# Optimization experiments

Measured on AMD Instinct MI355X. Metric: run time of the kernel, lower is better.

## Reference

```python
import jax, jax.numpy as jnp
import numpy as np

EPS = 1e-6


def _mp_match(reps, att, kernel):
    """BiMPM multi-perspective match.
    reps: (B,L,D); att: (B,L,D) or (B,1,D); kernel: (M,D).
    Returns (B,L,1+M): [tanh(sum(reps*att)), tanh(sum_d reps*kernel_m*att)].
    """
    prod = reps * att                                   # (B,L,D)
    cos = jnp.tanh(jnp.sum(prod, axis=-1, keepdims=True))   # (B,L,1)
    mp = jnp.tanh(jnp.einsum('bld,md->blm', prod, kernel))  # (B,L,M)
    return jnp.concatenate([cos, mp], axis=-1)


def setup_inputs() -> dict:
    key = jax.random.key(0)
    ks = jax.random.split(key, 12)
    B, Llt, Lrt, D, M, A = 32, 128, 128, 512, 64, 128
    H = D // 2
    u = lambda k, shape: jax.random.uniform(k, shape, jnp.float32, -0.05, 0.05)  # keras 'uniform' init
    return {
        'reps_lt': jax.random.normal(ks[0], (B, Llt, D), jnp.float32),
        'h_lt_fw': jax.random.normal(ks[1], (B, H), jnp.float32),
        'h_lt_bw': jax.random.normal(ks[2], (B, H), jnp.float32),
        'reps_rt': jax.random.normal(ks[3], (B, Lrt, D), jnp.float32),
        'h_rt_fw': jax.random.normal(ks[4], (B, H), jnp.float32),
        'h_rt_bw': jax.random.normal(ks[5], (B, H), jnp.float32),
        'kernel_full': u(ks[6], (M, D)),
        'kernel_mpool': u(ks[7], (M, D)),
        'attn_w1': u(ks[8], (D, A)),
        'diag_w': u(ks[9], (A,)),
        'kernel_att': u(ks[10], (M, D)),
        'kernel_maxatt': u(ks[11], (M, D)),
    }


def reference(reps_lt, h_lt_fw, h_lt_bw, reps_rt, h_rt_fw, h_rt_bw,
              kernel_full, kernel_mpool, attn_w1, diag_w,
              kernel_att, kernel_maxatt):
    # ---- full match: each left timestep vs last BiLSTM state of right ----
    h_rt = jnp.concatenate([h_rt_fw, h_rt_bw], axis=-1)[:, None, :]  # (B,1,D)
    full = _mp_match(reps_lt, h_rt, kernel_full)                     # (B,Ll,1+M)

    # ---- max-pooling match ----
    # t[b,r,l,m] = tanh(sum_d R[b,r,d]*K[m,d]*L[b,l,d]); max over right positions r
    r_scaled = jnp.einsum('brd,md->brmd', reps_rt, kernel_mpool)     # (B,Lr,M,D)
    t = jnp.tanh(jnp.einsum('brmd,bld->brlm', r_scaled, reps_lt))    # (B,Lr,Ll,M)
    mpool = jnp.max(t, axis=1)                                       # (B,Ll,M)

    # ---- attentive match ----
    a_lt = jnp.tanh(reps_lt @ attn_w1) * diag_w                      # (B,Ll,A)
    a_rt = jnp.tanh(reps_rt @ attn_w1)                               # (B,Lr,A)
    scores = jnp.einsum('bla,bra->blr', a_lt, a_rt)                  # (B,Ll,Lr)
    probs = jax.nn.softmax(scores, axis=-1)
    att = jnp.einsum('blr,brd->bld', probs, reps_rt)                 # (B,Ll,D)
    attentive = _mp_match(reps_lt, att, kernel_att)                  # (B,Ll,1+M)

    # ---- max-attentive match ----
    num = jnp.einsum('bld,brd->blr', reps_lt, reps_rt)
    n_lt = jnp.sqrt(jnp.maximum(jnp.sum(reps_lt * reps_lt, -1), EPS))[:, :, None]
    n_rt = jnp.sqrt(jnp.maximum(jnp.sum(reps_rt * reps_rt, -1), EPS))[:, None, :]
    rel = num / n_rt / n_lt                                          # (B,Ll,Lr)
    idx = jnp.argmax(rel, axis=2)                                    # (B,Ll) int
    max_att = jnp.take_along_axis(reps_rt, idx[:, :, None], axis=1)  # (B,Ll,D)
    maxatt = _mp_match(reps_lt, max_att, kernel_maxatt)              # (B,Ll,1+M)

    return jnp.concatenate([full, mpool, attentive, maxatt], axis=-1)  # (B,Ll,3+4M)
```

## Files before the change

### kernel.cpp

```cpp
#include <hip/hip_runtime.h>
#include <hip/hip_bf16.h>
#include <math.h>
#include <stdint.h>

typedef __attribute__((ext_vector_type(8))) short short8;
typedef __attribute__((ext_vector_type(4))) float float4v;

#define DEV static __device__ __forceinline__

DEV float bflo(unsigned int u) { union { unsigned int i; float f; } v; v.i = u << 16; return v.f; }
DEV float bfhi(unsigned int u) { union { unsigned int i; float f; } v; v.i = u & 0xffff0000u; return v.f; }
DEV unsigned short f2bf(float f) {
    union { float f; unsigned int i; } v; v.f = f;
    unsigned int x = v.i;
    return (unsigned short)((x + 0x7fffu + ((x >> 16) & 1u)) >> 16);
}
DEV unsigned int pack2(float a, float b) { return (unsigned int)f2bf(a) | ((unsigned int)f2bf(b) << 16); }
#if __has_builtin(__builtin_amdgcn_cvt_pk_bf16_f32)
DEV unsigned int pack2_fast(float a, float b) {
    typedef __attribute__((ext_vector_type(2))) short short2v;
    short2v r = __builtin_amdgcn_cvt_pk_bf16_f32(a, b);
    union { short2v s; unsigned int u; } v; v.s = r; return v.u;
}
#else
DEV unsigned int pack2_fast(float a, float b) { return pack2(a, b); }
#endif
DEV void unpack8(uint4 u, float* f) {
    f[0]=bflo(u.x); f[1]=bfhi(u.x); f[2]=bflo(u.y); f[3]=bfhi(u.y);
    f[4]=bflo(u.z); f[5]=bfhi(u.z); f[6]=bflo(u.w); f[7]=bfhi(u.w);
}

DEV void async16(const unsigned short* g, unsigned short* l) {
    __builtin_amdgcn_global_load_lds(
        (const __attribute__((address_space(1))) unsigned int*)g,
        (__attribute__((address_space(3))) unsigned int*)l, 16, 0, 0);
}

__global__ __launch_bounds__(256) void prep_kernel(const float* __restrict__ lt,
                                                   const float* __restrict__ rt,
                                                   const float* __restrict__ kf,
                                                   const float* __restrict__ kmp,
                                                   const float* __restrict__ ka,
                                                   const float* __restrict__ km,
                                                   const float* __restrict__ w1,
                                                   unsigned short* __restrict__ ltb,
                                                   unsigned short* __restrict__ rtb,
                                                   unsigned short* __restrict__ kb,
                                                   unsigned short* __restrict__ w1t,
                                                   double* __restrict__ rsq) {
    __shared__ double ws2[2][2];
    __shared__ float tile[32][33];
    int bid = blockIdx.x, t = threadIdx.x;
    if (bid < 4096) {
        bool isRt = bid >= 2048;
        int rl = t >> 7;
        int c  = t & 127;
        int row = (isRt ? (bid - 2048) : bid) * 2 + rl;
        const float* src = (isRt ? rt : lt) + (size_t)row * 512;
        unsigned short* dst = (isRt ? rtb : ltb) + (size_t)row * 512;
        float4 v = *(const float4*)(src + c * 4);
        ushort4 o;
        o.x = f2bf(v.x); o.y = f2bf(v.y); o.z = f2bf(v.z); o.w = f2bf(v.w);
        *(ushort4*)(dst + c * 4) = o;
        if (isRt) {
            double s = (double)v.x * v.x + (double)v.y * v.y
                     + (double)v.z * v.z + (double)v.w * v.w;
            #pragma unroll
            for (int off = 1; off < 64; off <<= 1) s += __shfl_xor(s, off, 64);
            if ((c & 63) == 0) ws2[rl][c >> 6] = s;
            __syncthreads();
            if (c == 0) rsq[row] = 1.0 / sqrt(ws2[rl][0] + ws2[rl][1]);
        }
    } else if (bid < 4224) {
        int kbk = bid - 4096;
        int ksel = kbk >> 5;
        const float* src = (ksel == 0) ? kf : (ksel == 1) ? kmp : (ksel == 2) ? ka : km;
        int off = (kbk & 31) * 1024 + t * 4;
        float4 v = *(const float4*)(src + off);
        ushort4 o;
        o.x = f2bf(v.x); o.y = f2bf(v.y); o.z = f2bf(v.z); o.w = f2bf(v.w);
        *(ushort4*)(kb + ksel * 32768 + off) = o;
    } else {
        int b2 = bid - 4224;
        int d0 = (b2 & 15) * 32, a0 = (b2 >> 4) * 32;
        int r = t >> 5, c = t & 31;
        #pragma unroll
        for (int i = 0; i < 32; i += 8)
            tile[r + i][c] = w1[(size_t)(d0 + r + i) * 128 + a0 + c];
        __syncthreads();
        #pragma unroll
        for (int i = 0; i < 32; i += 8)
            w1t[(size_t)(a0 + r + i) * 512 + d0 + c] = f2bf(tile[c][r + i]);
    }
}

__global__ __launch_bounds__(256, 3) void uber_kernel(
        const unsigned short* __restrict__ ltb,
        const unsigned short* __restrict__ rtb,
        const unsigned short* __restrict__ kmb,
        const unsigned short* __restrict__ w1t,
        const float* __restrict__ diag,
        unsigned short* __restrict__ a_all,
        const float* __restrict__ ltf,
        const float* __restrict__ rtf,
        const double* __restrict__ rsq,
        int* __restrict__ idxout,
        float* __restrict__ out) {
    __shared__ __align__(16) unsigned char smem[52224];
    int bx = blockIdx.x;
    int t = threadIdx.x;
    int wave = t >> 6, lane = t & 63;
    int q = lane >> 4, col = lane & 15, kq = q * 8;

    if (bx < 2048) {
        int xcd = bx & 7, jj = bx >> 3;
        int b = xcd * 4 + (jj >> 6);
        int m = jj & 63;
        unsigned short (*ltS)[72] = (unsigned short(*)[72])smem;
        unsigned short* rtL = (unsigned short*)(smem + 18432);
        float (*mx)[2] = (float(*)[2])(smem + 18432 + 32768);
        int wl = wave & 1, wr = wave >> 1;
        const unsigned short* ltp = ltb + (size_t)b * 65536;
        const unsigned short* rtp = rtb + (size_t)b * 65536;
        const unsigned short* kr = kmb + (size_t)m * 512;
        int srow = t >> 3, cg8 = t & 7, cg = cg8 * 8;
        int gsw = (cg8 ^ (srow & 7)) * 8;
        int wbase = (t & ~63) * 8;

        #pragma unroll
        for (int it = 0; it < 4; ++it)
            async16(rtp + (size_t)(it * 32 + srow) * 512 + gsw,
                    rtL + it * 2048 + wbase);
        uint4 pk = *(const uint4*)(kr + cg);
        uint4 plt[4];
        #pragma unroll
        for (int it = 0; it < 4; ++it)
            plt[it] = *(const uint4*)(ltp + (size_t)(it * 32 + srow) * 512 + cg);

        float4v acc[4][4] = {};
        for (int k0i = 0; k0i < 8; ++k0i) {
            float kf8[8]; unpack8(pk, kf8);
            #pragma unroll
            for (int it = 0; it < 4; ++it) {
                int row = it * 32 + srow;
                float lf[8]; unpack8(plt[it], lf);
                uint4 s;
                s.x = pack2_fast(lf[0] * kf8[0], lf[1] * kf8[1]);
                s.y = pack2_fast(lf[2] * kf8[2], lf[3] * kf8[3]);
                s.z = pack2_fast(lf[4] * kf8[4], lf[5] * kf8[5]);
                s.w = pack2_fast(lf[6] * kf8[6], lf[7] * kf8[7]);
                *(uint4*)&ltS[row][cg] = s;
            }
            __syncthreads();
            if (k0i < 7) {
                int k0n = (k0i + 1) * 64;
                int bofs = ((k0i + 1) & 1) * 8192;
                #pragma unroll
                for (int it = 0; it < 4; ++it)
                    async16(rtp + (size_t)(it * 32 + srow) * 512 + k0n + gsw,
                            rtL + bofs + it * 2048 + wbase);
                pk = *(const uint4*)(kr + k0n + cg);
                #pragma unroll
                for (int it = 0; it < 4; ++it)
                    plt[it] = *(const uint4*)(ltp + (size_t)(it * 32 + srow) * 512 + k0n + cg);
            }
            const unsigned short* rb = rtL + (k0i & 1) * 8192;
            #pragma unroll
            for (int kk = 0; kk < 64; kk += 32) {
                short8 af[4], bfr[4];
                #pragma unroll
                for (int i = 0; i < 4; ++i)
                    af[i] = *(const short8*)&ltS[wl * 64 + i * 16 + col][kk + kq];
                #pragma unroll
                for (int j = 0; j < 4; ++j) {
                    int row = wr * 64 + j * 16 + col;
                    int slot = ((kk >> 3) + q) ^ (row & 7);
                    bfr[j] = *(const short8*)&rb[row * 64 + slot * 8];
                }
                #pragma unroll
                for (int i = 0; i < 4; ++i)
                    #pragma unroll
                    for (int j = 0; j < 4; ++j)
                        acc[i][j] = __builtin_amdgcn_mfma_f32_16x16x32_bf16(af[i], bfr[j], acc[i][j], 0, 0, 0);
            }
            __syncthreads();
        }
        #pragma unroll
        for (int i = 0; i < 4; ++i)
            #pragma unroll
            for (int ii = 0; ii < 4; ++ii) {
                float v = fmaxf(fmaxf(acc[i][0][ii], acc[i][1][ii]), fmaxf(acc[i][2][ii], acc[i][3][ii]));
                #pragma unroll
                for (int off = 1; off < 16; off <<= 1) v = fmaxf(v, __shfl_xor(v, off, 64));
                if (col == 0) mx[wl * 64 + i * 16 + q * 4 + ii][wr] = v;
            }
        __syncthreads();
        if (t < 128)
            out[((size_t)(b * 128 + t)) * 259 + 65 + m] = tanhf(fmaxf(mx[t][0], mx[t][1]));

    } else if (bx < 2560) {
        int idA = bx - 2048;
        int xcd = idA & 7, jj = idA >> 3;
        int b = xcd * 4 + (jj >> 4);
        int L0 = (jj & 15) * 8;
        float* ltS = (float*)smem;
        float* buf = (float*)(smem + 16384);
        double* dvs = (double*)(smem + 49152);
        float* wv1 = (float*)(smem + 49152 + 128);
        float* wv2 = wv1 + 16;
        int* wi1 = (int*)(wv2 + 16);
        int* wi2 = wi1 + 16;
        int* candi = wi2 + 16;
        {
            int row = t >> 5, c0 = (t & 31) * 16;
            const float* src = ltf + ((size_t)(b * 128 + L0 + row)) * 512 + c0;
            #pragma unroll
            for (int i = 0; i < 4; ++i)
                *(float4*)&ltS[row * 512 + c0 + i * 4] = *(const float4*)(src + i * 4);
        }
        int lg = t >> 7;
        int rg = (t >> 2) & 31;
        int ds = t & 3;
        float acc[4][4] = {{0.f}};
        for (int p = 0; p < 8; ++p) {
            __syncthreads();
            {
                int row = t >> 1, c0 = (t & 1) * 32;
                const float* src = rtf + ((size_t)(b * 128 + row)) * 512 + p * 64 + c0;
                float f[32];
                #pragma unroll
                for (int i = 0; i < 8; ++i)
                    *(float4*)&f[i * 4] = *(const float4*)(src + i * 4);
                int base = row * 64;
                #pragma unroll
                for (int gg = 0; gg < 4; ++gg) {
                    int g = (t & 1) * 4 + gg;
                    int o = ((g ^ (row & 7)) * 8);
                    #pragma unroll
                    for (int k = 0; k < 8; ++k) buf[base + o + k] = f[gg * 8 + k];
                }
            }
            __syncthreads();
            #pragma unroll
            for (int sub = 0; sub < 2; ++sub) {
                int dloc = ds * 16 + sub * 8;
                int dglob = p * 64 + dloc;
                float a[4][8];
                #pragma unroll
                for (int i = 0; i < 4; ++i)
                    #pragma unroll
                    for (int k = 0; k < 8; ++k) a[i][k] = ltS[(lg * 4 + i) * 512 + dglob + k];
                int g = dloc >> 3;
                #pragma unroll
                for (int j = 0; j < 4; ++j) {
                    int r = rg + j * 32;
                    const float* rp = &buf[r * 64 + ((g ^ (r & 7)) * 8)];
                    float rv[8];
                    #pragma unroll
                    for (int k = 0; k < 8; ++k) rv[k] = rp[k];
                    #pragma unroll
                    for (int i = 0; i < 4; ++i)
                        #pragma unroll
                        for (int k = 0; k < 8; ++k)
                            acc[i][j] = fmaf(a[i][k], rv[k], acc[i][j]);
                }
            }
        }
        #pragma unroll
        for (int i = 0; i < 4; ++i)
            #pragma unroll
            for (int j = 0; j < 4; ++j) {
                acc[i][j] += __shfl_xor(acc[i][j], 1, 64);
                acc[i][j] += __shfl_xor(acc[i][j], 2, 64);
            }
        float v1[4], v2[4]; int i1[4], i2[4];
        #pragma unroll
        for (int i = 0; i < 4; ++i) {
            v1[i] = -3.0e38f; v2[i] = -3.0e38f; i1[i] = 0; i2[i] = 1;
            #pragma unroll
            for (int j = 0; j < 4; ++j) {
                int r = rg + j * 32;
                float s = acc[i][j] * (float)rsq[b * 128 + r];
                if (s > v1[i]) { v2[i] = v1[i]; i2[i] = i1[i]; v1[i] = s; i1[i] = r; }
                else if (s > v2[i]) { v2[i] = s; i2[i] = r; }
            }
        }
        #pragma unroll
        for (int off = 4; off < 64; off <<= 1) {
            #pragma unroll
            for (int i = 0; i < 4; ++i) {
                float u1 = __shfl_xor(v1[i], off, 64); int j1 = __shfl_xor(i1[i], off, 64);
                float u2 = __shfl_xor(v2[i], off, 64); int j2 = __shfl_xor(i2[i], off, 64);
                if (u1 > v1[i]) {
                    float ov = v1[i]; int oi = i1[i];
                    v1[i] = u1; i1[i] = j1;
                    if (u2 > ov) { v2[i] = u2; i2[i] = j2; } else { v2[i] = ov; i2[i] = oi; }
                } else if (u1 > v2[i]) { v2[i] = u1; i2[i] = j1; }
            }
        }
        if (lane == 0) {
            #pragma unroll
            for (int i = 0; i < 4; ++i) {
                int l = lg * 4 + i, h = wave & 1;
                wv1[l * 2 + h] = v1[i]; wi1[l * 2 + h] = i1[i];
                wv2[l * 2 + h] = v2[i]; wi2[l * 2 + h] = i2[i];
            }
        }
        __syncthreads();
        if (t < 8) {
            float a1 = wv1[t * 2], a2 = wv2[t * 2]; int ai1 = wi1[t * 2], ai2 = wi2[t * 2];
            float b1 = wv1[t * 2 + 1], b2 = wv2[t * 2 + 1]; int bi1 = wi1[t * 2 + 1], bi2 = wi2[t * 2 + 1];
            int ri1, ri2;
            if (b1 > a1) {
                ri1 = bi1;
                if (b2 > a1) { ri2 = bi2; } else { ri2 = ai1; }
            } else {
                ri1 = ai1;
                if (b1 > a2) { ri2 = bi1; } else { ri2 = ai2; }
            }
            candi[t * 2] = ri1; candi[t * 2 + 1] = ri2;
            (void)a2; (void)b2; (void)ai2; (void)bi2;
        }
        __syncthreads();
        {
            int dotid = t >> 4;
            int sub = t & 15;
            int l = dotid >> 1, c = dotid & 1;
            int r = candi[l * 2 + c];
            const float* lrow = ltf + ((size_t)(b * 128 + L0 + l)) * 512;
            const float* rrow = rtf + ((size_t)(b * 128 + r)) * 512;
            double s = 0.0;
            #pragma unroll 8
            for (int k = 0; k < 32; ++k) {
                int d = sub * 32 + k;
                s = fma((double)lrow[d], (double)rrow[d], s);
            }
            #pragma unroll
            for (int off = 1; off < 16; off <<= 1) s += __shfl_xor(s, off, 64);
            if (sub == 0) dvs[l * 2 + c] = s * rsq[b * 128 + r];
        }
        __syncthreads();
        if (t < 8) {
            int ia = candi[t * 2], ib = candi[t * 2 + 1];
            double va = dvs[t * 2], vb = dvs[t * 2 + 1];
            int res = (vb > va || (vb == va && ib < ia)) ? ib : ia;
            idxout[b * 128 + L0 + t] = res;
        }

    } else {
        int R0 = (bx - 2560) * 32;
        unsigned short (*aS)[72] = (unsigned short(*)[72])smem;
        unsigned short (*bS)[72] = (unsigned short(*)[72])(smem + 4608);
        float* diagS = (float*)(smem + 4608 + 18432);
        int wl = wave & 1, wr = wave >> 1;
        if (t < 128) diagS[t] = diag[t];
        const unsigned short* src = (R0 < 4096) ? (ltb + (size_t)R0 * 512) : (rtb + (size_t)(R0 - 4096) * 512);
        float4v acc[4] = {};
        for (int k0 = 0; k0 < 512; k0 += 64) {
            {
                int row = t >> 3, cg = (t & 7) * 8;
                *(uint4*)&aS[row][cg] = *(const uint4*)(src + (size_t)row * 512 + k0 + cg);
            }
            #pragma unroll
            for (int it = 0; it < 4; ++it) {
                int id = it * 256 + t;
                int row = id >> 3, cg = (id & 7) * 8;
                *(uint4*)&bS[row][cg] = *(const uint4*)(w1t + (size_t)row * 512 + k0 + cg);
            }
            __syncthreads();
            #pragma unroll
            for (int kk = 0; kk < 64; kk += 32) {
                short8 af = *(const short8*)&aS[wl * 16 + col][kk + kq];
                #pragma unroll
                for (int j = 0; j < 4; ++j) {
                    short8 bf = *(const short8*)&bS[wr * 64 + j * 16 + col][kk + kq];
                    acc[j] = __builtin_amdgcn_mfma_f32_16x16x32_bf16(af, bf, acc[j], 0, 0, 0);
                }
            }
            __syncthreads();
        }
        bool isLt = (R0 < 4096);
        #pragma unroll
        for (int j = 0; j < 4; ++j)
            #pragma unroll
            for (int ii = 0; ii < 4; ++ii) {
                int rowl = wl * 16 + q * 4 + ii;
                int n = wr * 64 + j * 16 + col;
                float v = tanhf(acc[j][ii]);
                if (isLt) v *= diagS[n];
                a_all[((size_t)(R0 + rowl)) * 128 + n] = f2bf(v);
            }
    }
}

__global__ __launch_bounds__(512, 2) void attn_kernel(const unsigned short* __restrict__ a_all,
                                                      const unsigned short* __restrict__ rtb,
                                                      unsigned short* __restrict__ attw) {
    int b = blockIdx.x, lg = blockIdx.y;
    int L0 = lg * 16;
    __shared__ __align__(16) unsigned short altS[16][136];
    __shared__ __align__(16) unsigned short artS[128][136];
    __shared__ __align__(16) unsigned short rtS[16][512];
    __shared__ float P[16][132];
    __shared__ float pmax[16][8];
    __shared__ float psum[16][8];
    int t = threadIdx.x;
    int wave = t >> 6, lane = t & 63;
    int q = lane >> 4, col = lane & 15, kq = q * 8;

    if (t < 256) {
        int row = t >> 4, c0 = (t & 15) * 8;
        *(uint4*)&altS[row][c0] = *(const uint4*)(a_all + ((size_t)(b * 128 + L0 + row)) * 128 + c0);
    }
    {
        int row = t >> 2, c0 = (t & 3) * 32;
        const unsigned short* src = a_all + ((size_t)(4096 + b * 128 + row)) * 128 + c0;
        #pragma unroll
        for (int i = 0; i < 4; ++i)
            *(uint4*)&artS[row][c0 + i * 8] = *(const uint4*)(src + i * 8);
    }
    __syncthreads();

    float4v acc = {};
    #pragma unroll
    for (int kk = 0; kk < 128; kk += 32) {
        short8 af = *(const short8*)&altS[col][kk + kq];
        short8 bf = *(const short8*)&artS[wave * 16 + col][kk + kq];
        acc = __builtin_amdgcn_mfma_f32_16x16x32_bf16(af, bf, acc, 0, 0, 0);
    }
    float m4[4], p4[4];
    #pragma unroll
    for (int ii = 0; ii < 4; ++ii) {
        float v = acc[ii];
        #pragma unroll
        for (int off = 1; off < 16; off <<= 1) v = fmaxf(v, __shfl_xor(v, off, 64));
        m4[ii] = v;
    }
    if (col == 0) {
        #pragma unroll
        for (int ii = 0; ii < 4; ++ii) pmax[q * 4 + ii][wave] = m4[ii];
    }
    __syncthreads();
    #pragma unroll
    for (int ii = 0; ii < 4; ++ii) {
        float M = pmax[q * 4 + ii][0];
        #pragma unroll
        for (int w = 1; w < 8; ++w) M = fmaxf(M, pmax[q * 4 + ii][w]);
        p4[ii] = expf(acc[ii] - M);
        float s = p4[ii];
        #pragma unroll
        for (int off = 1; off < 16; off <<= 1) s += __shfl_xor(s, off, 64);
        m4[ii] = s;
    }
    if (col == 0) {
        #pragma unroll
        for (int ii = 0; ii < 4; ++ii) psum[q * 4 + ii][wave] = m4[ii];
    }
    __syncthreads();
    #pragma unroll
    for (int ii = 0; ii < 4; ++ii) {
        float S = psum[q * 4 + ii][0] + psum[q * 4 + ii][1] + psum[q * 4 + ii][2] + psum[q * 4 + ii][3]
                + psum[q * 4 + ii][4] + psum[q * 4 + ii][5] + psum[q * 4 + ii][6] + psum[q * 4 + ii][7];
        P[q * 4 + ii][wave * 16 + col] = p4[ii] / S;
    }

    int l = t >> 5, cd = t & 31;
    float a8[2][8] = {{0.f}};
    for (int rcb = 0; rcb < 128; rcb += 16) {
        __syncthreads();
        {
            int row = t >> 5, c0 = (t & 31) * 16;
            const unsigned short* src = rtb + ((size_t)(b * 128 + rcb + row)) * 512 + c0;
            *(uint4*)&rtS[row][c0] = *(const uint4*)src;
            *(uint4*)&rtS[row][c0 + 8] = *(const uint4*)(src + 8);
        }
        __syncthreads();
        for (int rr = 0; rr < 16; ++rr) {
            float pr = P[l][rcb + rr];
            #pragma unroll
            for (int pass = 0; pass < 2; ++pass) {
                uint4 u = *(const uint4*)&rtS[rr][pass * 256 + cd * 8];
                float f[8]; unpack8(u, f);
                #pragma unroll
                for (int k = 0; k < 8; ++k) a8[pass][k] += pr * f[k];
            }
        }
    }
    size_t grow = (size_t)(b * 128 + L0 + l);
    #pragma unroll
    for (int pass = 0; pass < 2; ++pass) {
        uint4 o;
        o.x = pack2(a8[pass][0], a8[pass][1]);
        o.y = pack2(a8[pass][2], a8[pass][3]);
        o.z = pack2(a8[pass][4], a8[pass][5]);
        o.w = pack2(a8[pass][6], a8[pass][7]);
        *(uint4*)(attw + grow * 512 + pass * 256 + cd * 8) = o;
    }
}

__global__ __launch_bounds__(256, 2) void mpmatch_kernel(const float* __restrict__ lt,
                                                         const unsigned short* __restrict__ rtb,
                                                         const float* __restrict__ hfw,
                                                         const float* __restrict__ hbw,
                                                         const unsigned short* __restrict__ kb,
                                                         const unsigned short* __restrict__ attw,
                                                         const int* __restrict__ idxp,
                                                         float* __restrict__ out) {
    int lg = blockIdx.x, b = blockIdx.y, mode = blockIdx.z;
    int L0 = lg * 16;
    __shared__ __align__(16) unsigned short prods[16][520];
    __shared__ __align__(16) unsigned short Ks[32][520];
    __shared__ float red[4][2][16][17];
    int t = threadIdx.x;
    int wave = t >> 6, lane = t & 63;
    int q = lane >> 4, col = lane & 15, kq = q * 8;

    const unsigned short* Kp = kb + (size_t)((mode == 0) ? 0 : (mode == 1) ? 2 * 32768 : 3 * 32768);
    int obase = (mode == 0) ? 0 : (mode == 1) ? 129 : 194;

    int l = t >> 4, c = t & 15;
    int grow = b * 128 + L0 + l;
    const float* ltrow = lt + (size_t)grow * 512;
    const unsigned short* avrow = 0;
    if (mode == 1) avrow = attw + (size_t)grow * 512;
    else if (mode == 2) avrow = rtb + ((size_t)(b * 128 + idxp[grow])) * 512;

    float csum = 0.f;
    #pragma unroll
    for (int pass = 0; pass < 4; ++pass) {
        int d0 = pass * 128 + c * 8;
        float lf[8], af[8], pf[8];
        *(float4*)&lf[0] = *(const float4*)(ltrow + d0);
        *(float4*)&lf[4] = *(const float4*)(ltrow + d0 + 4);
        if (mode == 0) {
            const float* h = (d0 < 256) ? (hfw + b * 256 + d0) : (hbw + b * 256 + d0 - 256);
            *(float4*)&af[0] = *(const float4*)h;
            *(float4*)&af[4] = *(const float4*)(h + 4);
        } else {
            uint4 av = *(const uint4*)(avrow + d0);
            unpack8(av, af);
        }
        #pragma unroll
        for (int k = 0; k < 8; ++k) { pf[k] = lf[k] * af[k]; csum += pf[k]; }
        uint4 o;
        o.x = pack2(pf[0], pf[1]); o.y = pack2(pf[2], pf[3]);
        o.z = pack2(pf[4], pf[5]); o.w = pack2(pf[6], pf[7]);
        *(uint4*)&prods[l][d0] = o;
    }
    #pragma unroll
    for (int off = 1; off < 16; off <<= 1) csum += __shfl_xor(csum, off, 64);
    if (c == 0) out[(size_t)grow * 259 + obase] = tanhf(csum);

    for (int half = 0; half < 2; ++half) {
        {
            int row = t >> 3, c0 = (t & 7) * 64;
            const unsigned short* src = Kp + ((size_t)(half * 32 + row)) * 512 + c0;
            #pragma unroll
            for (int i = 0; i < 8; ++i)
                *(uint4*)&Ks[row][c0 + i * 8] = *(const uint4*)(src + i * 8);
        }
        __syncthreads();
        float4v acc[2] = {};
        #pragma unroll
        for (int kk = 0; kk < 128; kk += 32) {
            short8 af = *(const short8*)&prods[col][wave * 128 + kk + kq];
            #pragma unroll
            for (int j = 0; j < 2; ++j) {
                short8 bf = *(const short8*)&Ks[j * 16 + col][wave * 128 + kk + kq];
                acc[j] = __builtin_amdgcn_mfma_f32_16x16x32_bf16(af, bf, acc[j], 0, 0, 0);
            }
        }
        #pragma unroll
        for (int j = 0; j < 2; ++j)
            #pragma unroll
            for (int ii = 0; ii < 4; ++ii)
                red[wave][j][q * 4 + ii][col] = acc[j][ii];
        __syncthreads();
        for (int o = t; o < 512; o += 256) {
            int ll = o >> 5, jm = o & 31;
            int j = jm >> 4, mc = jm & 15;
            float s = red[0][j][ll][mc] + red[1][j][ll][mc] + red[2][j][ll][mc] + red[3][j][ll][mc];
            out[((size_t)(b * 128 + L0 + ll)) * 259 + obase + 1 + half * 32 + jm] = tanhf(s);
        }
        __syncthreads();
    }
}

extern "C" void kernel_launch(void* const* d_in, const int* in_sizes, int n_in,
                              void* d_out, int out_size, void* d_ws, size_t ws_size,
                              hipStream_t stream) {
    const float* lt  = (const float*)d_in[0];
    const float* rt  = (const float*)d_in[3];
    const float* hfw = (const float*)d_in[4];
    const float* hbw = (const float*)d_in[5];
    const float* kf  = (const float*)d_in[6];
    const float* kmp = (const float*)d_in[7];
    const float* w1  = (const float*)d_in[8];
    const float* dia = (const float*)d_in[9];
    const float* ka  = (const float*)d_in[10];
    const float* km  = (const float*)d_in[11];
    float* out = (float*)d_out;

    char* wsb = (char*)d_ws;
    unsigned short* ltb16 = (unsigned short*)(wsb);
    unsigned short* rtb16 = (unsigned short*)(wsb + 4194304);
    unsigned short* kb16  = (unsigned short*)(wsb + 8388608);
    unsigned short* w1t   = (unsigned short*)(wsb + 8650752);
    unsigned short* a_all = (unsigned short*)(wsb + 8781824);
    unsigned short* attw  = (unsigned short*)(wsb + 10878976);
    double*         rsq   = (double*)(wsb + 15073280);
    int*            idx   = (int*)(wsb + 15106048);

    prep_kernel<<<4288, 256, 0, stream>>>(lt, rt, kf, kmp, ka, km, w1, ltb16, rtb16, kb16, w1t, rsq);
    uber_kernel<<<2816, 256, 0, stream>>>(ltb16, rtb16, kb16 + 32768, w1t, dia, a_all,
                                          lt, rt, rsq, idx, out);
    attn_kernel<<<dim3(32, 8), 512, 0, stream>>>(a_all, rtb16, attw);
    mpmatch_kernel<<<dim3(8, 32, 3), 256, 0, stream>>>(lt, rtb16, hfw, hbw, kb16, attw, idx, out);
}
```

Baseline: 197.2 us.

## Fuse attentive multi-perspective match into attention kernel; double-buffer mpool LHS tile

The attentive match (product of reps_lt with the attention-weighted vector, then cosine and per-perspective projections) now runs inside attn_kernel. This removes the attw bf16 round-trip through global memory, and mpmatch drops to two modes. Separately, the max-pool path of uber_kernel double-buffers the scaled-left shared tile, so the next chunk is built while MFMAs run on the current one. That change raises shared memory use and lowers the occupancy hint from 3 to 2 blocks, and attn_kernel also drops to 1 block per CU.

Result: slower. 218.6 us (+10.9%).

```diff
diff --git a/kernel.cpp b/kernel.cpp
--- a/kernel.cpp
+++ b/kernel.cpp
@@ -94,7 +94,7 @@
     }
 }
 
-__global__ __launch_bounds__(256, 3) void uber_kernel(
+__global__ __launch_bounds__(256, 2) void uber_kernel(
         const unsigned short* __restrict__ ltb,
         const unsigned short* __restrict__ rtb,
         const unsigned short* __restrict__ kmb,
@@ -106,7 +106,7 @@
         const double* __restrict__ rsq,
         int* __restrict__ idxout,
         float* __restrict__ out) {
-    __shared__ __align__(16) unsigned char smem[52224];
+    __shared__ __align__(16) unsigned char smem[70656];
     int bx = blockIdx.x;
     int t = threadIdx.x;
     int wave = t >> 6, lane = t & 63;
@@ -116,9 +116,9 @@
         int xcd = bx & 7, jj = bx >> 3;
         int b = xcd * 4 + (jj >> 6);
         int m = jj & 63;
-        unsigned short (*ltS)[72] = (unsigned short(*)[72])smem;
-        unsigned short* rtL = (unsigned short*)(smem + 18432);
-        float (*mx)[2] = (float(*)[2])(smem + 18432 + 32768);
+        unsigned short (*ltS)[128][72] = (unsigned short(*)[128][72])smem;
+        unsigned short* rtL = (unsigned short*)(smem + 36864);
+        float (*mx)[2] = (float(*)[2])(smem + 69632);
         int wl = wave & 1, wr = wave >> 1;
         const unsigned short* ltp = ltb + (size_t)b * 65536;
         const unsigned short* rtp = rtb + (size_t)b * 65536;
@@ -127,50 +127,69 @@
         int gsw = (cg8 ^ (srow & 7)) * 8;
         int wbase = (t & ~63) * 8;
 
+        uint4 pkB = *(const uint4*)(kr + cg);
+        uint4 pltB[4];
+        #pragma unroll
+        for (int it = 0; it < 4; ++it)
+            pltB[it] = *(const uint4*)(ltp + (size_t)(it * 32 + srow) * 512 + cg);
         #pragma unroll
         for (int it = 0; it < 4; ++it)
             async16(rtp + (size_t)(it * 32 + srow) * 512 + gsw,
                     rtL + it * 2048 + wbase);
-        uint4 pk = *(const uint4*)(kr + cg);
-        uint4 plt[4];
-        #pragma unroll
-        for (int it = 0; it < 4; ++it)
-            plt[it] = *(const uint4*)(ltp + (size_t)(it * 32 + srow) * 512 + cg);
-
-        float4v acc[4][4] = {};
-        for (int k0i = 0; k0i < 8; ++k0i) {
-            float kf8[8]; unpack8(pk, kf8);
+        {
+            float kf8[8]; unpack8(pkB, kf8);
             #pragma unroll
             for (int it = 0; it < 4; ++it) {
-                int row = it * 32 + srow;
-                float lf[8]; unpack8(plt[it], lf);
+                float lf[8]; unpack8(pltB[it], lf);
                 uint4 s;
                 s.x = pack2_fast(lf[0] * kf8[0], lf[1] * kf8[1]);
                 s.y = pack2_fast(lf[2] * kf8[2], lf[3] * kf8[3]);
                 s.z = pack2_fast(lf[4] * kf8[4], lf[5] * kf8[5]);
                 s.w = pack2_fast(lf[6] * kf8[6], lf[7] * kf8[7]);
-                *(uint4*)&ltS[row][cg] = s;
-            }
-            __syncthreads();
-            if (k0i < 7) {
-                int k0n = (k0i + 1) * 64;
-                int bofs = ((k0i + 1) & 1) * 8192;
+                *(uint4*)&ltS[0][it * 32 + srow][cg] = s;
+            }
+        }
+        pkB = *(const uint4*)(kr + 64 + cg);
+        #pragma unroll
+        for (int it = 0; it < 4; ++it)
+            pltB[it] = *(const uint4*)(ltp + (size_t)(it * 32 + srow) * 512 + 64 + cg);
+        __syncthreads();
+
+        float4v acc[4][4] = {};
+        for (int i = 0; i < 8; ++i) {
+            int cur = i & 1, nxt = cur ^ 1;
+            if (i < 7) {
+                int k0n = (i + 1) * 64;
                 #pragma unroll
                 for (int it = 0; it < 4; ++it)
                     async16(rtp + (size_t)(it * 32 + srow) * 512 + k0n + gsw,
-                            rtL + bofs + it * 2048 + wbase);
-                pk = *(const uint4*)(kr + k0n + cg);
-                #pragma unroll
-                for (int it = 0; it < 4; ++it)
-                    plt[it] = *(const uint4*)(ltp + (size_t)(it * 32 + srow) * 512 + k0n + cg);
-            }
-            const unsigned short* rb = rtL + (k0i & 1) * 8192;
+                            rtL + nxt * 8192 + it * 2048 + wbase);
+                float kf8[8]; unpack8(pkB, kf8);
+                #pragma unroll
+                for (int it = 0; it < 4; ++it) {
+                    float lf[8]; unpack8(pltB[it], lf);
+                    uint4 s;
+                    s.x = pack2_fast(lf[0] * kf8[0], lf[1] * kf8[1]);
+                    s.y = pack2_fast(lf[2] * kf8[2], lf[3] * kf8[3]);
+                    s.z = pack2_fast(lf[4] * kf8[4], lf[5] * kf8[5]);
+                    s.w = pack2_fast(lf[6] * kf8[6], lf[7] * kf8[7]);
+                    *(uint4*)&ltS[nxt][it * 32 + srow][cg] = s;
+                }
+                if (i < 6) {
+                    int k0n2 = (i + 2) * 64;
+                    pkB = *(const uint4*)(kr + k0n2 + cg);
+                    #pragma unroll
+                    for (int it = 0; it < 4; ++it)
+                        pltB[it] = *(const uint4*)(ltp + (size_t)(it * 32 + srow) * 512 + k0n2 + cg);
+                }
+            }
+            const unsigned short* rb = rtL + cur * 8192;
             #pragma unroll
             for (int kk = 0; kk < 64; kk += 32) {
                 short8 af[4], bfr[4];
                 #pragma unroll
-                for (int i = 0; i < 4; ++i)
-                    af[i] = *(const short8*)&ltS[wl * 64 + i * 16 + col][kk + kq];
+                for (int i4 = 0; i4 < 4; ++i4)
+                    af[i4] = *(const short8*)&ltS[cur][wl * 64 + i4 * 16 + col][kk + kq];
                 #pragma unroll
                 for (int j = 0; j < 4; ++j) {
                     int row = wr * 64 + j * 16 + col;
@@ -178,10 +197,10 @@
                     bfr[j] = *(const short8*)&rb[row * 64 + slot * 8];
                 }
                 #pragma unroll
-                for (int i = 0; i < 4; ++i)
+                for (int i4 = 0; i4 < 4; ++i4)
                     #pragma unroll
                     for (int j = 0; j < 4; ++j)
-                        acc[i][j] = __builtin_amdgcn_mfma_f32_16x16x32_bf16(af[i], bfr[j], acc[i][j], 0, 0, 0);
+                        acc[i4][j] = __builtin_amdgcn_mfma_f32_16x16x32_bf16(af[i4], bfr[j], acc[i4][j], 0, 0, 0);
             }
             __syncthreads();
         }
@@ -393,14 +412,17 @@
     }
 }
 
-__global__ __launch_bounds__(512, 2) void attn_kernel(const unsigned short* __restrict__ a_all,
+__global__ __launch_bounds__(512, 1) void attn_kernel(const unsigned short* __restrict__ a_all,
                                                       const unsigned short* __restrict__ rtb,
-                                                      unsigned short* __restrict__ attw) {
+                                                      const float* __restrict__ ltf,
+                                                      const unsigned short* __restrict__ kb_att,
+                                                      float* __restrict__ out) {
     int b = blockIdx.x, lg = blockIdx.y;
     int L0 = lg * 16;
     __shared__ __align__(16) unsigned short altS[16][136];
     __shared__ __align__(16) unsigned short artS[128][136];
     __shared__ __align__(16) unsigned short rtS[16][512];
+    __shared__ __align__(16) unsigned short prodsF[16][520];
     __shared__ float P[16][132];
     __shared__ float pmax[16][8];
     __shared__ float psum[16][8];
@@ -486,15 +508,64 @@
             }
         }
     }
-    size_t grow = (size_t)(b * 128 + L0 + l);
+
+    int grow = b * 128 + L0 + l;
+    const float* ltrow = ltf + (size_t)grow * 512;
+    float csum = 0.f;
     #pragma unroll
     for (int pass = 0; pass < 2; ++pass) {
+        int d0 = pass * 256 + cd * 8;
+        float lf[8];
+        *(float4*)&lf[0] = *(const float4*)(ltrow + d0);
+        *(float4*)&lf[4] = *(const float4*)(ltrow + d0 + 4);
+        float pf[8];
+        #pragma unroll
+        for (int k = 0; k < 8; ++k) { pf[k] = lf[k] * a8[pass][k]; csum += pf[k]; }
         uint4 o;
-        o.x = pack2(a8[pass][0], a8[pass][1]);
-        o.y = pack2(a8[pass][2], a8[pass][3]);
-        o.z = pack2(a8[pass][4], a8[pass][5]);
-        o.w = pack2(a8[pass][6], a8[pass][7]);
-        *(uint4*)(attw + grow * 512 + pass * 256 + cd * 8) = o;
+        o.x = pack2(pf[0], pf[1]); o.y = pack2(pf[2], pf[3]);
+        o.z = pack2(pf[4], pf[5]); o.w = pack2(pf[6], pf[7]);
+        *(uint4*)&prodsF[l][d0] = o;
+    }
+    #pragma unroll
+    for (int off = 1; off < 32; off <<= 1) csum += __shfl_xor(csum, off, 64);
+    if (cd == 0) out[(size_t)grow * 259 + 129] = tanhf(csum);
+
+    unsigned short* Ks = &artS[0][0];
+    float* red = (float*)&rtS[0][0];
+    for (int half = 0; half < 2; ++half) {
+        __syncthreads();
+        {
+            int row = t >> 4, c0 = (t & 15) * 32;
+            const unsigned short* src = kb_att + ((size_t)(half * 32 + row)) * 512 + c0;
+            #pragma unroll
+            for (int i = 0; i < 4; ++i)
+                *(uint4*)&Ks[row * 520 + c0 + i * 8] = *(const uint4*)(src + i * 8);
+        }
+        __syncthreads();
+        float4v pacc[2] = {};
+        #pragma unroll
+        for (int kk = 0; kk < 64; kk += 32) {
+            short8 af = *(const short8*)&prodsF[col][wave * 64 + kk + kq];
+            #pragma unroll
+            for (int j = 0; j < 2; ++j) {
+                short8 bf = *(const short8*)&Ks[(j * 16 + col) * 520 + wave * 64 + kk + kq];
+                pacc[j] = __builtin_amdgcn_mfma_f32_16x16x32_bf16(af, bf, pacc[j], 0, 0, 0);
+            }
+        }
+        #pragma unroll
+        for (int j = 0; j < 2; ++j)
+            #pragma unroll
+            for (int ii = 0; ii < 4; ++ii)
+                red[((wave * 2 + j) * 16 + q * 4 + ii) * 16 + col] = pacc[j][ii];
+        __syncthreads();
+        {
+            int ll = t >> 5, jm = t & 31;
+            int j = jm >> 4, mc = jm & 15;
+            float s = 0.f;
+            #pragma unroll
+            for (int w = 0; w < 8; ++w) s += red[((w * 2 + j) * 16 + ll) * 16 + mc];
+            out[((size_t)(b * 128 + L0 + ll)) * 259 + 130 + half * 32 + jm] = tanhf(s);
+        }
     }
 }
 
@@ -503,10 +574,9 @@
                                                          const float* __restrict__ hfw,
                                                          const float* __restrict__ hbw,
                                                          const unsigned short* __restrict__ kb,
-                                                         const unsigned short* __restrict__ attw,
                                                          const int* __restrict__ idxp,
                                                          float* __restrict__ out) {
-    int lg = blockIdx.x, b = blockIdx.y, mode = blockIdx.z;
+    int lg = blockIdx.x, b = blockIdx.y, mode = blockIdx.z ? 2 : 0;
     int L0 = lg * 16;
     __shared__ __align__(16) unsigned short prods[16][520];
     __shared__ __align__(16) unsigned short Ks[32][520];
@@ -515,15 +585,14 @@
     int wave = t >> 6, lane = t & 63;
     int q = lane >> 4, col = lane & 15, kq = q * 8;
 
-    const unsigned short* Kp = kb + (size_t)((mode == 0) ? 0 : (mode == 1) ? 2 * 32768 : 3 * 32768);
-    int obase = (mode == 0) ? 0 : (mode == 1) ? 129 : 194;
+    const unsigned short* Kp = kb + (size_t)((mode == 0) ? 0 : 3 * 32768);
+    int obase = (mode == 0) ? 0 : 194;
 
     int l = t >> 4, c = t & 15;
     int grow = b * 128 + L0 + l;
     const float* ltrow = lt + (size_t)grow * 512;
     const unsigned short* avrow = 0;
-    if (mode == 1) avrow = attw + (size_t)grow * 512;
-    else if (mode == 2) avrow = rtb + ((size_t)(b * 128 + idxp[grow])) * 512;
+    if (mode == 2) avrow = rtb + ((size_t)(b * 128 + idxp[grow])) * 512;
 
     float csum = 0.f;
     #pragma unroll
@@ -607,13 +676,12 @@
     unsigned short* kb16  = (unsigned short*)(wsb + 8388608);
     unsigned short* w1t   = (unsigned short*)(wsb + 8650752);
     unsigned short* a_all = (unsigned short*)(wsb + 8781824);
-    unsigned short* attw  = (unsigned short*)(wsb + 10878976);
     double*         rsq   = (double*)(wsb + 15073280);
     int*            idx   = (int*)(wsb + 15106048);
 
     prep_kernel<<<4288, 256, 0, stream>>>(lt, rt, kf, kmp, ka, km, w1, ltb16, rtb16, kb16, w1t, rsq);
     uber_kernel<<<2816, 256, 0, stream>>>(ltb16, rtb16, kb16 + 32768, w1t, dia, a_all,
                                           lt, rt, rsq, idx, out);
-    attn_kernel<<<dim3(32, 8), 512, 0, stream>>>(a_all, rtb16, attw);
-    mpmatch_kernel<<<dim3(8, 32, 3), 256, 0, stream>>>(lt, rtb16, hfw, hbw, kb16, attw, idx, out);
-}
+    attn_kernel<<<dim3(32, 8), 512, 0, stream>>>(a_all, rtb16, lt, kb16 + 2 * 32768, out);
+    mpmatch_kernel<<<dim3(8, 32, 2), 256, 0, stream>>>(lt, rtb16, hfw, hbw, kb16, idx, out);
+}
```
